# Optimization experiments

Measured on AMD Instinct MI355X. Metric: run time of the kernel, lower is better.

The kernel has to match this reference:

```python
import jax, jax.numpy as jnp
import numpy as np

B, L, A, F = 4096, 12, 768, 4096  # batch, n_layers, d_activations, d_features


def setup_inputs() -> dict:
    key = jax.random.key(0)
    k_x, k_enc, k_dec, k_m, k_s = jax.random.split(key, 5)
    x = jax.random.normal(k_x, (B, L, A), dtype=jnp.float32)
    # Encoder: uniform(-1/sqrt(F), 1/sqrt(F)) per reset_parameters
    enc_thresh = 1.0 / np.sqrt(F)
    W_enc = jax.random.uniform(k_enc, (L, A, F), jnp.float32, -enc_thresh, enc_thresh)
    # Decoder: triangular weights W_i of shape (i+1, F, A), packed along axis 0.
    # Total rows = L*(L+1)//2. uniform(-1/sqrt(A*L), 1/sqrt(A*L)).
    dec_thresh = 1.0 / np.sqrt(A * L)
    n_tri = L * (L + 1) // 2
    W_dec_packed = jax.random.uniform(k_dec, (n_tri, F, A), jnp.float32, -dec_thresh, dec_thresh)
    # JumpReLU threshold per (layer, feature), init 0.03
    theta = jnp.full((L, F), 0.03, dtype=jnp.float32)
    # Dimensionwise input standardizer stats (per layer, per activation dim)
    in_mean = 0.1 * jax.random.normal(k_m, (L, A), dtype=jnp.float32)
    in_std = 1.0 + 0.1 * jax.random.uniform(k_s, (L, A), dtype=jnp.float32)
    return {"x": x, "in_mean": in_mean, "in_std": in_std, "W_enc": W_enc,
            "theta": theta, "W_dec_packed": W_dec_packed}


def reference(x, in_mean, in_std, W_enc, theta, W_dec_packed):
    # Input standardization: (x - mean) / std, broadcast over batch
    sx = (x - in_mean[None]) / in_std[None]                      # [B, L, A]
    # Encoder: per-layer dense projection
    enc = jnp.einsum('bla,laf->blf', sx, W_enc)                  # [B, L, F]
    # JumpReLU: x * (x > theta)
    act = enc * (enc > theta[None]).astype(enc.dtype)            # [B, L, F]
    # Decoder: triangular accumulation. Layer i reads features of layers 0..i
    # with its own weight tensor W_i (slice of the packed triangular buffer).
    n_layers = W_enc.shape[0]
    preds = []
    off = 0
    for i in range(n_layers):
        W_i = W_dec_packed[off:off + i + 1]                      # [i+1, F, A]
        preds.append(jnp.einsum('blf,lfa->ba', act[:, :i + 1], W_i))
        off += i + 1
    logits = jnp.stack(preds, axis=1)                            # [B, L, A]
    # Original forward returns (logits, encoder_out, concat_w_dec); the
    # concat_w_dec list is just a reshape of the decoder params, omitted here.
    return logits, enc
```

## Files before the change

### kernel.cpp

```cpp
#include <hip/hip_runtime.h>
#include <cstdint>
#include <cstddef>

#define B_ 4096
#define L_ 12
#define A_ 768
#define F_ 4096
#define NTRI 78

typedef __bf16 bf16x8 __attribute__((ext_vector_type(8)));
typedef float f32x4 __attribute__((ext_vector_type(4)));
typedef unsigned short u16x4 __attribute__((ext_vector_type(4)));
typedef unsigned short u16x8 __attribute__((ext_vector_type(8)));

__device__ __forceinline__ unsigned short f32_to_bf16(float f) {
  unsigned int u = __float_as_uint(f);
  u += 0x7fffu + ((u >> 16) & 1u);
  return (unsigned short)(u >> 16);
}

__device__ __forceinline__ void gload_lds16(const void* g, void* l) {
  __builtin_amdgcn_global_load_lds(
      (const __attribute__((address_space(1))) void*)g,
      (__attribute__((address_space(3))) void*)l,
      16, 0, 0);
}

__global__ __launch_bounds__(256) void prep_sx(
    const float* __restrict__ x, const float* __restrict__ mean,
    const float* __restrict__ stdv, unsigned short* __restrict__ sx) {
  size_t i4 = (size_t)blockIdx.x * 256 + threadIdx.x;
  size_t e = i4 * 4;
  if (e >= (size_t)B_ * L_ * A_) return;
  unsigned int a = (unsigned int)(e % A_);
  unsigned int t = (unsigned int)(e / A_);
  unsigned int b = t / L_;
  unsigned int l = t % L_;
  float4 xv = *(const float4*)(x + e);
  float4 mv = *(const float4*)(mean + (size_t)l * A_ + a);
  float4 sv = *(const float4*)(stdv + (size_t)l * A_ + a);
  u16x4 o;
  o.x = f32_to_bf16((xv.x - mv.x) / sv.x);
  o.y = f32_to_bf16((xv.y - mv.y) / sv.y);
  o.z = f32_to_bf16((xv.z - mv.z) / sv.z);
  o.w = f32_to_bf16((xv.w - mv.w) / sv.w);
  *(u16x4*)(sx + ((size_t)l * B_ + b) * A_ + a) = o;
}

__global__ __launch_bounds__(256) void transpose_cvt64(
    const float* __restrict__ in, unsigned short* __restrict__ out,
    int R, int C) {
  __shared__ float tile[64][65];
  const float* inz = in + (size_t)blockIdx.z * R * C;
  unsigned short* outz = out + (size_t)blockIdx.z * R * C;
  const int c0 = blockIdx.x * 64, r0 = blockIdx.y * 64;
  const int t = threadIdx.x;
  {
    const int c = (t & 15) * 4;
    const int rb = t >> 4;
#pragma unroll
    for (int q = 0; q < 4; ++q) {
      const int r = rb + q * 16;
      float4 v = *(const float4*)(inz + (size_t)(r0 + r) * C + (c0 + c));
      tile[r][c] = v.x; tile[r][c + 1] = v.y;
      tile[r][c + 2] = v.z; tile[r][c + 3] = v.w;
    }
  }
  __syncthreads();
  {
    const int c = t >> 2;
    const int rb = (t & 3) * 16;
#pragma unroll
    for (int h = 0; h < 2; ++h) {
      u16x8 o;
#pragma unroll
      for (int j = 0; j < 8; ++j) o[j] = f32_to_bf16(tile[rb + h * 8 + j][c]);
      *(u16x8*)(outz + (size_t)(c0 + c) * R + (r0 + rb + h * 8)) = o;
    }
  }
}

__device__ __forceinline__ bf16x8 read_frag(const char* base, int row, int g) {
  int ss = g ^ ((row >> 1) & 3);
  return *(const bf16x8*)(base + row * 64 + ss * 16);
}

template <class FSrc>
__device__ __forceinline__ void stage_tile(FSrc src, int kt, char* ringbase,
                                           int w, int lane) {
  char* base = ringbase + (kt & 3) * 16384;
#pragma unroll
  for (int q = 0; q < 2; ++q) {
    int c = q * 8 + w;
    int row = c * 16 + (lane >> 2);
    int ss = (lane & 3) ^ ((row >> 1) & 3);
    gload_lds16(src(kt, row, ss * 8), base + c * 1024);
  }
}

template <class FA, class FB>
__device__ __forceinline__ void gemm_core(int KT, char* AS, char* BS, int w,
                                          int lane, int wr, int wc, FA srcA,
                                          FB srcB, f32x4 (&acc)[8][4]) {
  const int g = lane >> 4;
  const int fr = lane & 15;
  stage_tile(srcA, 0, AS, w, lane);
  stage_tile(srcB, 0, BS, w, lane);
  stage_tile(srcA, 1, AS, w, lane);
  stage_tile(srcB, 1, BS, w, lane);
  stage_tile(srcA, 2, AS, w, lane);
  stage_tile(srcB, 2, BS, w, lane);
  asm volatile("s_waitcnt vmcnt(8)" ::: "memory");
  __builtin_amdgcn_s_barrier();

  bf16x8 bcur[4], a0cur[4], a1[4], bnxt[4], a0nxt[4];
#pragma unroll
  for (int ni = 0; ni < 4; ++ni)
    bcur[ni] = read_frag(BS, wc * 64 + ni * 16 + fr, g);
#pragma unroll
  for (int mi = 0; mi < 4; ++mi)
    a0cur[mi] = read_frag(AS, wr * 128 + mi * 16 + fr, g);

  for (int kt = 0; kt < KT; ++kt) {
    const char* Ab = AS + (kt & 3) * 16384;
    const char* Bb = BS + (kt & 3) * 16384;
    const char* Abn = AS + ((kt + 1) & 3) * 16384;
    const char* Bbn = BS + ((kt + 1) & 3) * 16384;
    if (kt + 2 < KT) { asm volatile("s_waitcnt vmcnt(4)" ::: "memory"); }
    else             { asm volatile("s_waitcnt vmcnt(0)" ::: "memory"); }
    __builtin_amdgcn_s_barrier();
#pragma unroll
    for (int mi = 0; mi < 4; ++mi)
      a1[mi] = read_frag(Ab, wr * 128 + (mi + 4) * 16 + fr, g);
    if (kt + 3 < KT) {
      stage_tile(srcA, kt + 3, AS, w, lane);
      stage_tile(srcB, kt + 3, BS, w, lane);
    }
    __builtin_amdgcn_s_setprio(1);
#pragma unroll
    for (int mi = 0; mi < 4; ++mi)
#pragma unroll
      for (int ni = 0; ni < 4; ++ni)
        acc[mi][ni] = __builtin_amdgcn_mfma_f32_16x16x32_bf16(
            a0cur[mi], bcur[ni], acc[mi][ni], 0, 0, 0);
    __builtin_amdgcn_s_setprio(0);
    if (kt + 1 < KT) {
#pragma unroll
      for (int ni = 0; ni < 4; ++ni)
        bnxt[ni] = read_frag(Bbn, wc * 64 + ni * 16 + fr, g);
#pragma unroll
      for (int mi = 0; mi < 4; ++mi)
        a0nxt[mi] = read_frag(Abn, wr * 128 + mi * 16 + fr, g);
    }
    __builtin_amdgcn_s_setprio(1);
#pragma unroll
    for (int mi = 0; mi < 4; ++mi)
#pragma unroll
      for (int ni = 0; ni < 4; ++ni)
        acc[mi + 4][ni] = __builtin_amdgcn_mfma_f32_16x16x32_bf16(
            a1[mi], bcur[ni], acc[mi + 4][ni], 0, 0, 0);
    __builtin_amdgcn_s_setprio(0);
#pragma unroll
    for (int q = 0; q < 4; ++q) {
      bcur[q] = bnxt[q];
      a0cur[q] = a0nxt[q];
    }
  }
}

__global__ __launch_bounds__(512, 2) void enc_gemm8(
    const unsigned short* __restrict__ sxT,
    const unsigned short* __restrict__ wT,
    const float* __restrict__ theta,
    float* __restrict__ enc_out,
    unsigned short* __restrict__ act)
{
  extern __shared__ __align__(16) char lds[];
  char* AS = lds;
  char* BS = lds + 65536;
  const int b = blockIdx.x;
  const int wg = (b & 7) * 384 + (b >> 3);
  const int l = wg >> 8;
  const int blk = wg & 255;
  const int m0 = (blk & 15) * 256;
  const int n0 = (blk >> 4) * 256;
  const int tid = threadIdx.x;
  const int w = tid >> 6, lane = tid & 63;
  const int wr = w >> 2, wc = w & 3;

  f32x4 acc[8][4] = {};
  auto srcA = [&](int kt, int row, int ce) {
    return sxT + ((size_t)l * B_ + m0 + row) * A_ + kt * 32 + ce;
  };
  auto srcB = [&](int kt, int row, int ce) {
    return wT + ((size_t)l * F_ + n0 + row) * A_ + kt * 32 + ce;
  };
  gemm_core(A_ / 32, AS, BS, w, lane, wr, wc, srcA, srcB, acc);

  const int g = lane >> 4, fr = lane & 15;
#pragma unroll
  for (int ni = 0; ni < 4; ++ni) {
    const int gcol = n0 + wc * 64 + ni * 16 + fr;
    const float th = theta[(size_t)l * F_ + gcol];
#pragma unroll
    for (int mi = 0; mi < 8; ++mi) {
      const int growb = m0 + wr * 128 + mi * 16 + g * 4;
#pragma unroll
      for (int jj = 0; jj < 4; ++jj) {
        const float v = acc[mi][ni][jj];
        const size_t grow = (size_t)(growb + jj);
        enc_out[(grow * L_ + l) * F_ + gcol] = v;
        act[((size_t)l * B_ + grow) * F_ + gcol] =
            (v > th) ? f32_to_bf16(v) : (unsigned short)0;
      }
    }
  }
}

__global__ __launch_bounds__(512, 2) void dec_gemm8(
    const unsigned short* __restrict__ act,
    const unsigned short* __restrict__ wdecT,
    float* __restrict__ logits)
{
  extern __shared__ __align__(16) char lds[];
  char* AS = lds;
  char* BS = lds + 65536;
  const int b = blockIdx.x;
  const int xcd = b & 7;
  const int idx = b >> 3;
  const int z = idx / 6;
  const int j = idx - z * 6;
  const int i = 11 - z;
  const int blk = xcd * 6 + j;
  const int m0 = (blk & 15) * 256;
  const int n0 = (blk >> 4) * 256;
  const int triBase = i * (i + 1) / 2;
  const int KT = (i + 1) * 128;
  const int tid = threadIdx.x;
  const int w = tid >> 6, lane = tid & 63;
  const int wr = w >> 2, wc = w & 3;

  f32x4 acc[8][4] = {};
  auto srcA = [&](int kt, int row, int ce) {
    int l = kt >> 7;
    int kk0 = (kt & 127) * 32;
    return act + ((size_t)l * B_ + m0 + row) * F_ + kk0 + ce;
  };
  auto srcB = [&](int kt, int row, int ce) {
    int l = kt >> 7;
    int kk0 = (kt & 127) * 32;
    return wdecT + ((size_t)(triBase + l) * A_ + n0 + row) * F_ + kk0 + ce;
  };
  gemm_core(KT, AS, BS, w, lane, wr, wc, srcA, srcB, acc);

  const int g = lane >> 4, fr = lane & 15;
#pragma unroll
  for (int mi = 0; mi < 8; ++mi) {
    const int growb = m0 + wr * 128 + mi * 16 + g * 4;
#pragma unroll
    for (int ni = 0; ni < 4; ++ni) {
      const int gcol = n0 + wc * 64 + ni * 16 + fr;
#pragma unroll
      for (int jj = 0; jj < 4; ++jj)
        logits[((size_t)(growb + jj) * L_ + i) * A_ + gcol] = acc[mi][ni][jj];
    }
  }
}

extern "C" void kernel_launch(void* const* d_in, const int* in_sizes, int n_in,
                              void* d_out, int out_size, void* d_ws,
                              size_t ws_size, hipStream_t stream) {
  (void)in_sizes; (void)n_in; (void)out_size; (void)ws_size;
  const float* x = (const float*)d_in[0];
  const float* mean = (const float*)d_in[1];
  const float* stdv = (const float*)d_in[2];
  const float* Wenc = (const float*)d_in[3];
  const float* theta = (const float*)d_in[4];
  const float* Wdec = (const float*)d_in[5];

  float* logits = (float*)d_out;
  float* enc = (float*)d_out + (size_t)B_ * L_ * A_;

  char* ws = (char*)d_ws;
  const size_t actBytes = (size_t)L_ * B_ * F_ * 2;
  const size_t sxBytes = (size_t)L_ * B_ * A_ * 2;
  unsigned short* act = (unsigned short*)ws;
  unsigned short* sx = (unsigned short*)(ws + actBytes);
  unsigned short* wencT = (unsigned short*)(ws + actBytes + sxBytes);
  unsigned short* wdecT = (unsigned short*)(ws + actBytes);

  hipFuncSetAttribute((const void*)enc_gemm8,
                      hipFuncAttributeMaxDynamicSharedMemorySize, 131072);
  hipFuncSetAttribute((const void*)dec_gemm8,
                      hipFuncAttributeMaxDynamicSharedMemorySize, 131072);

  prep_sx<<<(B_ * L_ * A_ / 4 + 255) / 256, 256, 0, stream>>>(x, mean, stdv, sx);
  transpose_cvt64<<<dim3(F_ / 64, A_ / 64, L_), 256, 0, stream>>>(
      Wenc, wencT, A_, F_);
  enc_gemm8<<<3072, 512, 131072, stream>>>(sx, wencT, theta, enc, act);
  transpose_cvt64<<<dim3(A_ / 64, F_ / 64, NTRI), 256, 0, stream>>>(
      Wdec, wdecT, F_, A_);
  dec_gemm8<<<576, 512, 131072, stream>>>(act, wdecT, logits);
}
```

Measured before the change: 2.960 ms.

## Restructure GEMM mainloop to 64-wide K tiles with interleaved double-buffered staging

Replaces the shared GEMM core with a K=64-per-stage version. It uses a two-slot LDS double buffer and an XOR swizzle over 8 groups of 16 bytes. Global-to-LDS loads for the next tile are split into an A half and a B half, interleaved between four MFMA phases separated by barriers. Per-lane global addresses are precomputed as base pointers plus 32-bit k offsets, and the decoder's XCD-aware block ordering is replaced by a linear mapping. The aim is to cut address arithmetic and loop overhead and to overlap loads with MFMA. In exchange, prefetch depth drops from a three-tile lookahead to one, barriers per iteration rise, and cache locality across XCDs may suffer.

```diff
diff --git a/kernel.cpp b/kernel.cpp
--- a/kernel.cpp
+++ b/kernel.cpp
@@ -80,91 +80,115 @@
   }
 }
 
-__device__ __forceinline__ bf16x8 read_frag(const char* base, int row, int g) {
-  int ss = g ^ ((row >> 1) & 3);
-  return *(const bf16x8*)(base + row * 64 + ss * 16);
-}
-
-template <class FSrc>
-__device__ __forceinline__ void stage_tile(FSrc src, int kt, char* ringbase,
-                                           int w, int lane) {
-  char* base = ringbase + (kt & 3) * 16384;
-#pragma unroll
-  for (int q = 0; q < 2; ++q) {
-    int c = q * 8 + w;
-    int row = c * 16 + (lane >> 2);
-    int ss = (lane & 3) ^ ((row >> 1) & 3);
-    gload_lds16(src(kt, row, ss * 8), base + c * 1024);
-  }
-}
-
-template <class FA, class FB>
-__device__ __forceinline__ void gemm_core(int KT, char* AS, char* BS, int w,
-                                          int lane, int wr, int wc, FA srcA,
-                                          FB srcB, f32x4 (&acc)[8][4]) {
+template <class KOffA, class KOffB>
+__device__ __forceinline__ void gemm_core64(
+    int KT, char* AS, char* BS,
+    const char* gA0, const char* gB0, int ldA, int ldB,
+    int w, int wr, int wc, int lane,
+    KOffA koffA, KOffB koffB, f32x4 (&acc)[8][4]) {
   const int g = lane >> 4;
   const int fr = lane & 15;
-  stage_tile(srcA, 0, AS, w, lane);
-  stage_tile(srcB, 0, BS, w, lane);
-  stage_tile(srcA, 1, AS, w, lane);
-  stage_tile(srcB, 1, BS, w, lane);
-  stage_tile(srcA, 2, AS, w, lane);
-  stage_tile(srcB, 2, BS, w, lane);
-  asm volatile("s_waitcnt vmcnt(8)" ::: "memory");
+  const int f7 = fr & 7;
+  const uint32_t aRow = (uint32_t)(wr * 128 + fr) * 128;
+  const uint32_t bRow = (uint32_t)(wc * 64 + fr) * 128;
+  const uint32_t c0 = (uint32_t)((g ^ f7) * 16);
+  const uint32_t c1 = (uint32_t)(((4 | g) ^ f7) * 16);
+  const uint32_t aOff0 = aRow + c0, aOff1 = aRow + c1;
+  const uint32_t bOff0 = bRow + c0, bOff1 = bRow + c1;
+
+  auto stageA = [&](int kt) {
+    uint32_t off = koffA(kt);
+    char* d = AS + ((kt & 1) << 15) + (w << 10);
+#pragma unroll
+    for (int q = 0; q < 4; ++q)
+      gload_lds16(gA0 + off + (uint32_t)q * 64u * (uint32_t)ldA, d + q * 8192);
+  };
+  auto stageB = [&](int kt) {
+    uint32_t off = koffB(kt);
+    char* d = BS + ((kt & 1) << 15) + (w << 10);
+#pragma unroll
+    for (int q = 0; q < 4; ++q)
+      gload_lds16(gB0 + off + (uint32_t)q * 64u * (uint32_t)ldB, d + q * 8192);
+  };
+
+  stageA(0);
+  stageB(0);
+  asm volatile("s_waitcnt vmcnt(0)" ::: "memory");
   __builtin_amdgcn_s_barrier();
 
-  bf16x8 bcur[4], a0cur[4], a1[4], bnxt[4], a0nxt[4];
-#pragma unroll
-  for (int ni = 0; ni < 4; ++ni)
-    bcur[ni] = read_frag(BS, wc * 64 + ni * 16 + fr, g);
-#pragma unroll
-  for (int mi = 0; mi < 4; ++mi)
-    a0cur[mi] = read_frag(AS, wr * 128 + mi * 16 + fr, g);
-
+  bf16x8 bk[4], aA[4], aB[4];
   for (int kt = 0; kt < KT; ++kt) {
-    const char* Ab = AS + (kt & 3) * 16384;
-    const char* Bb = BS + (kt & 3) * 16384;
-    const char* Abn = AS + ((kt + 1) & 3) * 16384;
-    const char* Bbn = BS + ((kt + 1) & 3) * 16384;
-    if (kt + 2 < KT) { asm volatile("s_waitcnt vmcnt(4)" ::: "memory"); }
-    else             { asm volatile("s_waitcnt vmcnt(0)" ::: "memory"); }
-    __builtin_amdgcn_s_barrier();
-#pragma unroll
-    for (int mi = 0; mi < 4; ++mi)
-      a1[mi] = read_frag(Ab, wr * 128 + (mi + 4) * 16 + fr, g);
-    if (kt + 3 < KT) {
-      stage_tile(srcA, kt + 3, AS, w, lane);
-      stage_tile(srcB, kt + 3, BS, w, lane);
-    }
+    const char* Ab = AS + ((kt & 1) << 15);
+    const char* Bb = BS + ((kt & 1) << 15);
+    const bool more = (kt + 1 < KT);
+#pragma unroll
+    for (int ni = 0; ni < 4; ++ni)
+      bk[ni] = *(const bf16x8*)(Bb + bOff0 + ni * 2048);
+#pragma unroll
+    for (int mi = 0; mi < 4; ++mi)
+      aA[mi] = *(const bf16x8*)(Ab + aOff0 + mi * 2048);
+    if (more) stageA(kt + 1);
+    asm volatile("" ::: "memory");
+    __builtin_amdgcn_s_barrier();
     __builtin_amdgcn_s_setprio(1);
 #pragma unroll
     for (int mi = 0; mi < 4; ++mi)
 #pragma unroll
       for (int ni = 0; ni < 4; ++ni)
         acc[mi][ni] = __builtin_amdgcn_mfma_f32_16x16x32_bf16(
-            a0cur[mi], bcur[ni], acc[mi][ni], 0, 0, 0);
+            aA[mi], bk[ni], acc[mi][ni], 0, 0, 0);
     __builtin_amdgcn_s_setprio(0);
-    if (kt + 1 < KT) {
-#pragma unroll
-      for (int ni = 0; ni < 4; ++ni)
-        bnxt[ni] = read_frag(Bbn, wc * 64 + ni * 16 + fr, g);
-#pragma unroll
-      for (int mi = 0; mi < 4; ++mi)
-        a0nxt[mi] = read_frag(Abn, wr * 128 + mi * 16 + fr, g);
-    }
+    asm volatile("" ::: "memory");
+    __builtin_amdgcn_s_barrier();
+#pragma unroll
+    for (int mi = 0; mi < 4; ++mi)
+      aB[mi] = *(const bf16x8*)(Ab + aOff0 + (4 + mi) * 2048);
+    if (more) stageB(kt + 1);
+    asm volatile("" ::: "memory");
+    __builtin_amdgcn_s_barrier();
     __builtin_amdgcn_s_setprio(1);
 #pragma unroll
     for (int mi = 0; mi < 4; ++mi)
 #pragma unroll
       for (int ni = 0; ni < 4; ++ni)
         acc[mi + 4][ni] = __builtin_amdgcn_mfma_f32_16x16x32_bf16(
-            a1[mi], bcur[ni], acc[mi + 4][ni], 0, 0, 0);
+            aB[mi], bk[ni], acc[mi + 4][ni], 0, 0, 0);
     __builtin_amdgcn_s_setprio(0);
-#pragma unroll
-    for (int q = 0; q < 4; ++q) {
-      bcur[q] = bnxt[q];
-      a0cur[q] = a0nxt[q];
-    }
+    asm volatile("" ::: "memory");
+    __builtin_amdgcn_s_barrier();
+#pragma unroll
+    for (int ni = 0; ni < 4; ++ni)
+      bk[ni] = *(const bf16x8*)(Bb + bOff1 + ni * 2048);
+#pragma unroll
+    for (int mi = 0; mi < 4; ++mi)
+      aA[mi] = *(const bf16x8*)(Ab + aOff1 + mi * 2048);
+    asm volatile("" ::: "memory");
+    __builtin_amdgcn_s_barrier();
+    __builtin_amdgcn_s_setprio(1);
+#pragma unroll
+    for (int mi = 0; mi < 4; ++mi)
+#pragma unroll
+      for (int ni = 0; ni < 4; ++ni)
+        acc[mi][ni] = __builtin_amdgcn_mfma_f32_16x16x32_bf16(
+            aA[mi], bk[ni], acc[mi][ni], 0, 0, 0);
+    __builtin_amdgcn_s_setprio(0);
+    asm volatile("" ::: "memory");
+    __builtin_amdgcn_s_barrier();
+#pragma unroll
+    for (int mi = 0; mi < 4; ++mi)
+      aB[mi] = *(const bf16x8*)(Ab + aOff1 + (4 + mi) * 2048);
+    asm volatile("" ::: "memory");
+    __builtin_amdgcn_s_barrier();
+    __builtin_amdgcn_s_setprio(1);
+#pragma unroll
+    for (int mi = 0; mi < 4; ++mi)
+#pragma unroll
+      for (int ni = 0; ni < 4; ++ni)
+        acc[mi + 4][ni] = __builtin_amdgcn_mfma_f32_16x16x32_bf16(
+            aB[mi], bk[ni], acc[mi + 4][ni], 0, 0, 0);
+    __builtin_amdgcn_s_setprio(0);
+    asm volatile("s_waitcnt vmcnt(0)" ::: "memory");
+    __builtin_amdgcn_s_barrier();
   }
 }
 
@@ -187,15 +211,19 @@
   const int tid = threadIdx.x;
   const int w = tid >> 6, lane = tid & 63;
   const int wr = w >> 2, wc = w & 3;
+  const int sg = (lane & 7) ^ (lane >> 3);
+  const int srow = w * 8 + (lane >> 3);
+
+  const char* gA0 = (const char*)sxT +
+      ((size_t)l * B_ + m0 + srow) * (A_ * 2) + sg * 16;
+  const char* gB0 = (const char*)wT +
+      ((size_t)l * F_ + n0 + srow) * (A_ * 2) + sg * 16;
 
   f32x4 acc[8][4] = {};
-  auto srcA = [&](int kt, int row, int ce) {
-    return sxT + ((size_t)l * B_ + m0 + row) * A_ + kt * 32 + ce;
-  };
-  auto srcB = [&](int kt, int row, int ce) {
-    return wT + ((size_t)l * F_ + n0 + row) * A_ + kt * 32 + ce;
-  };
-  gemm_core(A_ / 32, AS, BS, w, lane, wr, wc, srcA, srcB, acc);
+  auto koffA = [](int kt) { return (uint32_t)kt * 128u; };
+  auto koffB = [](int kt) { return (uint32_t)kt * 128u; };
+  gemm_core64(A_ / 64, AS, BS, gA0, gB0, A_ * 2, A_ * 2, w, wr, wc, lane,
+              koffA, koffB, acc);
 
   const int g = lane >> 4, fr = lane & 15;
 #pragma unroll
@@ -226,32 +254,34 @@
   char* AS = lds;
   char* BS = lds + 65536;
   const int b = blockIdx.x;
-  const int xcd = b & 7;
-  const int idx = b >> 3;
-  const int z = idx / 6;
-  const int j = idx - z * 6;
+  const int z = b / 48;
+  const int blk = b - z * 48;
   const int i = 11 - z;
-  const int blk = xcd * 6 + j;
   const int m0 = (blk & 15) * 256;
   const int n0 = (blk >> 4) * 256;
   const int triBase = i * (i + 1) / 2;
-  const int KT = (i + 1) * 128;
+  const int KT = (i + 1) * 64;
   const int tid = threadIdx.x;
   const int w = tid >> 6, lane = tid & 63;
   const int wr = w >> 2, wc = w & 3;
+  const int sg = (lane & 7) ^ (lane >> 3);
+  const int srow = w * 8 + (lane >> 3);
+
+  const char* gA0 = (const char*)act + ((size_t)(m0 + srow)) * (F_ * 2) + sg * 16;
+  const char* gB0 = (const char*)wdecT +
+      ((size_t)(triBase * A_ + n0 + srow)) * (F_ * 2) + sg * 16;
 
   f32x4 acc[8][4] = {};
-  auto srcA = [&](int kt, int row, int ce) {
-    int l = kt >> 7;
-    int kk0 = (kt & 127) * 32;
-    return act + ((size_t)l * B_ + m0 + row) * F_ + kk0 + ce;
+  auto koffA = [](int kt) {
+    return (uint32_t)(kt >> 6) * (uint32_t)(B_ * F_ * 2) +
+           (uint32_t)(kt & 63) * 128u;
   };
-  auto srcB = [&](int kt, int row, int ce) {
-    int l = kt >> 7;
-    int kk0 = (kt & 127) * 32;
-    return wdecT + ((size_t)(triBase + l) * A_ + n0 + row) * F_ + kk0 + ce;
+  auto koffB = [](int kt) {
+    return (uint32_t)(kt >> 6) * (uint32_t)(A_ * F_ * 2) +
+           (uint32_t)(kt & 63) * 128u;
   };
-  gemm_core(KT, AS, BS, w, lane, wr, wc, srcA, srcB, acc);
+  gemm_core64(KT, AS, BS, gA0, gB0, F_ * 2, F_ * 2, w, wr, wc, lane,
+              koffA, koffB, acc);
 
   const int g = lane >> 4, fr = lane & 15;
 #pragma unroll
```

After: 2.826 ms. 4.5% less time.
